# Kernel optimization log

Measured on AMD Instinct MI355X. Metric: run time of the kernel, lower is better.

Reference implementation:

```python
import jax, jax.numpy as jnp
import numpy as np

N, D, H, E = 32768, 1024, 1024, 4


def setup_inputs() -> dict:
    key = jax.random.key(0)
    ks = jax.random.split(key, 10)
    s = 0.02  # xavier-ish init scale for stability
    return {
        "features": jax.random.normal(ks[0], (N, D), dtype=jnp.float32),
        "symbol_ids": jax.random.randint(ks[1], (N,), 0, E, dtype=jnp.int32),
        "W1": jax.random.normal(ks[2], (E, D, H), dtype=jnp.float32) * s,
        "b1": jax.random.normal(ks[3], (E, H), dtype=jnp.float32) * s,
        "W2": jax.random.normal(ks[4], (E, H, H), dtype=jnp.float32) * s,
        "b2": jax.random.normal(ks[5], (E, H), dtype=jnp.float32) * s,
        "W3": jax.random.normal(ks[6], (E, H, 1), dtype=jnp.float32) * s,
        "b3": jax.random.normal(ks[7], (E, 1), dtype=jnp.float32) * s,
        "slope": jax.random.normal(ks[8], (E,), dtype=jnp.float32),
        "intercept": jax.random.normal(ks[9], (E,), dtype=jnp.float32),
    }


def reference(features, symbol_ids, W1, b1, W2, b2, W3, b3, slope, intercept):
    # Run every atom through every expert MLP (E is tiny), then select by symbol.
    # h1: [E, N, H]
    h = jax.nn.relu(jnp.einsum("nd,edh->enh", features, W1) + b1[:, None, :])
    h = jax.nn.relu(jnp.einsum("enh,ehk->enk", h, W2) + b2[:, None, :])
    y = (jnp.einsum("enk,eko->eno", h, W3) + b3[:, None, :])[..., 0]  # [E, N]
    per_atom = slope[:, None] * y + intercept[:, None]                # [E, N]
    sel = symbol_ids[None, :] == jnp.arange(E, dtype=symbol_ids.dtype)[:, None]
    atomic_energies = jnp.sum(jnp.where(sel, per_atom, 0.0), axis=0)  # [N]
    image_energy = jnp.sum(atomic_energies)                           # scalar
    return image_energy
```

## Files before the change

kernel.cpp:

```cpp
#include <hip/hip_runtime.h>
#include <hip/hip_bf16.h>
#include <stdint.h>

#define NATOMS 32768
#define DDIM   1024
#define HDIM   1024
#define ENUM   4
#define MCAP   (NATOMS + ENUM * 128)

typedef unsigned short u16;
typedef unsigned char  u8;
typedef __attribute__((ext_vector_type(8)))  int   i32x8;
typedef __attribute__((ext_vector_type(16))) float f32x16;
typedef __attribute__((ext_vector_type(4)))  float f32x4;

static const size_t XP_OFF   = 0;
static const size_t H1_OFF   = XP_OFF  + (size_t)MCAP * 1024;
static const size_t W1T_OFF  = H1_OFF  + (size_t)MCAP * 1024;
static const size_t W2T_OFF  = W1T_OFF + (size_t)ENUM * 1024 * 1024;
static const size_t PERM_OFF = W2T_OFF + (size_t)ENUM * 1024 * 1024;
static const size_t META_OFF = PERM_OFF + (size_t)MCAP * 4;

__device__ __forceinline__ u8 f2fp8(float x) {
    int w = __builtin_amdgcn_cvt_pk_fp8_f32(x, x, 0, false);
    return (u8)(w & 0xFF);
}

__global__ void k_init(int* __restrict__ perm, int* __restrict__ meta,
                       float* __restrict__ out) {
    int i = blockIdx.x * 256 + threadIdx.x;
    if (i < MCAP) perm[i] = -1;
    if (blockIdx.x == 0) {
        if (threadIdx.x < 256) meta[threadIdx.x] = 0;
        if (threadIdx.x == 0) out[0] = 0.0f;
    }
}

__global__ void k_count(const int* __restrict__ sym, int* __restrict__ meta) {
    int n = blockIdx.x * 256 + threadIdx.x;
    int lane = threadIdx.x & 63;
    int e = sym[n];
#pragma unroll
    for (int j = 0; j < ENUM; ++j) {
        unsigned long long mask = __ballot(e == j);
        if (mask) {
            int leader = __ffsll((long long)mask) - 1;
            if (lane == leader)
                atomicAdd(&meta[j * 16], __popcll(mask));
        }
    }
}

__global__ void k_offsets(int* __restrict__ meta, const float* __restrict__ slope,
                          const float* __restrict__ b3, const float* __restrict__ inter,
                          float* __restrict__ out) {
    if (threadIdx.x == 0 && blockIdx.x == 0) {
        int off = 0;
        float c = 0.f;
        for (int e = 0; e < 4; ++e) {
            meta[128 + e]    = off;
            meta[64 + e*16]  = off;
            int cnt = meta[e * 16];
            c += (float)cnt * (slope[e] * b3[e] + inter[e]);
            off += (cnt + 127) & ~127;
        }
        meta[132] = off;
        out[0] = c;
    }
}

__global__ void k_scatter(const int* __restrict__ sym, int* __restrict__ meta,
                          int* __restrict__ perm) {
    int n = blockIdx.x * 256 + threadIdx.x;
    int lane = threadIdx.x & 63;
    int e = sym[n];
#pragma unroll
    for (int j = 0; j < ENUM; ++j) {
        unsigned long long mask = __ballot(e == j);
        if (mask) {
            int leader = __ffsll((long long)mask) - 1;
            int base = 0;
            if (lane == leader)
                base = atomicAdd(&meta[64 + j * 16], __popcll(mask));
            base = __shfl(base, leader, 64);
            if (e == j) {
                int rank = __popcll(mask & ((1ull << lane) - 1ull));
                perm[base + rank] = n;
            }
        }
    }
}

__global__ void k_convx(const float* __restrict__ F, const int* __restrict__ perm,
                        u8* __restrict__ Xp) {
    int g = blockIdx.x * 256 + threadIdx.x;
    int slot = g >> 7, c = g & 127;
    int src = perm[slot];
    uint2 v;
    if (src < 0) {
        v.x = 0u; v.y = 0u;
    } else {
        const float* fp = F + (size_t)src * 1024 + c * 8;
        int w0 = 0, w1 = 0;
        w0 = __builtin_amdgcn_cvt_pk_fp8_f32(fp[0], fp[1], w0, false);
        w0 = __builtin_amdgcn_cvt_pk_fp8_f32(fp[2], fp[3], w0, true);
        w1 = __builtin_amdgcn_cvt_pk_fp8_f32(fp[4], fp[5], w1, false);
        w1 = __builtin_amdgcn_cvt_pk_fp8_f32(fp[6], fp[7], w1, true);
        v.x = (unsigned)w0; v.y = (unsigned)w1;
    }
    *(uint2*)(void*)(Xp + (size_t)g * 8) = v;
}

__global__ void k_transw(const float* __restrict__ W1, u8* __restrict__ W1T,
                         const float* __restrict__ W2, u8* __restrict__ W2T) {
    __shared__ u8 tile[64][65];
    const float* W  = blockIdx.z ? W2  : W1;
    u8*          WT = blockIdx.z ? W2T : W1T;
    int e  = blockIdx.y;
    int tn = blockIdx.x & 15;
    int tk = blockIdx.x >> 4;
    const float* Wp = W  + (size_t)e * 1024 * 1024;
    u8*         WTp = WT + (size_t)e * 1024 * 1024;
    int c = threadIdx.x & 63, r0 = threadIdx.x >> 6;
#pragma unroll
    for (int i = 0; i < 16; ++i) {
        int r = r0 + i * 4;
        tile[r][c] = f2fp8(32.0f * Wp[(size_t)(tk * 64 + r) * 1024 + tn * 64 + c]);
    }
    __syncthreads();
#pragma unroll
    for (int i = 0; i < 16; ++i) {
        int r = r0 + i * 4;
        WTp[(size_t)(tn * 64 + r) * 1024 + tk * 64 + c] = tile[c][r];
    }
}

template <bool FUSE>
__global__ __launch_bounds__(256, 4)
void k_gemm(const u8* __restrict__ A, const u8* __restrict__ BT,
            const float* __restrict__ bias, u8* __restrict__ C,
            const int* __restrict__ meta, const float* __restrict__ W3,
            const float* __restrict__ slope, float* __restrict__ out) {
    __shared__ u8 As[128 * 64];
    __shared__ u8 Bs[128 * 64];
    const int* offs = meta + 128;

    const int bx = blockIdx.x;
    const int by = blockIdx.y;
    const int m0 = by * 128, n0 = bx * 128;
    int e = (m0 >= offs[1]) + (m0 >= offs[2]) + (m0 >= offs[3]);

    const int t = threadIdx.x;
    const int w = t >> 6, lane = t & 63;
    const int l31 = lane & 31, khalf = lane >> 5;
    const int wm = w & 1, wn = w >> 1;

    const u8* Ag = A + (size_t)m0 * 1024;
    const u8* Bg = BT + (size_t)e * 1024 * 1024 + (size_t)n0 * 1024;

    const int srow   = t >> 2;
    const int gchunk = (t & 3) ^ (srow & 3);

    f32x16 acc[2][2] = {};

    for (int kt = 0; kt < 1024 / 64; ++kt) {
        const int kb = kt * 64;
#pragma unroll
        for (int i = 0; i < 2; ++i) {
            int row = i * 64 + srow;
            __builtin_amdgcn_global_load_lds(
                (const void*)(Ag + (size_t)row * 1024 + kb + gchunk * 16),
                (void*)(As + i * 4096 + w * 1024), 16, 0, 0);
        }
#pragma unroll
        for (int i = 0; i < 2; ++i) {
            int row = i * 64 + srow;
            __builtin_amdgcn_global_load_lds(
                (const void*)(Bg + (size_t)row * 1024 + kb + gchunk * 16),
                (void*)(Bs + i * 4096 + w * 1024), 16, 0, 0);
        }
        __syncthreads();

        i32x8 a[2], b[2];
#pragma unroll
        for (int mi = 0; mi < 2; ++mi) {
            int m = wm * 64 + mi * 32 + l31;
            const u8* base = As + m * 64 + ((khalf ^ ((m >> 1) & 1)) << 5);
            uint4 lo = *(const uint4*)(const void*)(base + ((m & 1) << 4));
            uint4 hi = *(const uint4*)(const void*)(base + (((m & 1) ^ 1) << 4));
            union { uint4 q[2]; i32x8 v; } u;
            u.q[0] = lo; u.q[1] = hi;
            a[mi] = u.v;
        }
#pragma unroll
        for (int ni = 0; ni < 2; ++ni) {
            int n = wn * 64 + ni * 32 + l31;
            const u8* base = Bs + n * 64 + ((khalf ^ ((n >> 1) & 1)) << 5);
            uint4 lo = *(const uint4*)(const void*)(base + ((n & 1) << 4));
            uint4 hi = *(const uint4*)(const void*)(base + (((n & 1) ^ 1) << 4));
            union { uint4 q[2]; i32x8 v; } u;
            u.q[0] = lo; u.q[1] = hi;
            b[ni] = u.v;
        }
#pragma unroll
        for (int mi = 0; mi < 2; ++mi)
#pragma unroll
            for (int ni = 0; ni < 2; ++ni)
                acc[mi][ni] = __builtin_amdgcn_mfma_scale_f32_32x32x64_f8f6f4(
                    a[mi], b[ni], acc[mi][ni],
                    0, 0,
                    0, 0x7F7F7F7F,
                    0, 0x7A7A7A7A);
        __syncthreads();
    }

    if (!FUSE) {
#pragma unroll
        for (int ni = 0; ni < 2; ++ni) {
            int col = n0 + wn * 64 + ni * 32 + l31;
            float bv = bias[e * 1024 + col];
#pragma unroll
            for (int mi = 0; mi < 2; ++mi) {
                int rowb = m0 + wm * 64 + mi * 32 + 4 * khalf;
#pragma unroll
                for (int reg = 0; reg < 16; ++reg) {
                    int rowg = rowb + (reg & 3) + 8 * (reg >> 2);
                    float v = acc[mi][ni][reg] + bv;
                    v = v > 0.f ? v : 0.f;
                    C[(size_t)rowg * 1024 + col] = f2fp8(v);
                }
            }
        }
    } else {
        const int segEnd = offs[e] + meta[e * 16];
        const float se = slope[e];
        float psum = 0.f;
#pragma unroll
        for (int ni = 0; ni < 2; ++ni) {
            int col = n0 + wn * 64 + ni * 32 + l31;
            float bv  = bias[e * 1024 + col];
            float w3s = W3[e * 1024 + col] * se;
#pragma unroll
            for (int mi = 0; mi < 2; ++mi) {
                int rowb = m0 + wm * 64 + mi * 32 + 4 * khalf;
#pragma unroll
                for (int reg = 0; reg < 16; ++reg) {
                    int rowg = rowb + (reg & 3) + 8 * (reg >> 2);
                    float v = acc[mi][ni][reg] + bv;
                    v = v > 0.f ? v : 0.f;
                    psum += (rowg < segEnd) ? v * w3s : 0.f;
                }
            }
        }
#pragma unroll
        for (int o = 32; o; o >>= 1) psum += __shfl_xor(psum, o, 64);
        float* red = (float*)As;
        if (lane == 0) red[w] = psum;
        __syncthreads();
        if (t == 0) atomicAdd(out, red[0] + red[1] + red[2] + red[3]);
    }
}

extern "C" void kernel_launch(void* const* d_in, const int* in_sizes, int n_in,
                              void* d_out, int out_size, void* d_ws, size_t ws_size,
                              hipStream_t stream) {
    const float* features = (const float*)d_in[0];
    const int*   sym      = (const int*)d_in[1];
    const float* W1       = (const float*)d_in[2];
    const float* b1       = (const float*)d_in[3];
    const float* W2       = (const float*)d_in[4];
    const float* b2       = (const float*)d_in[5];
    const float* W3       = (const float*)d_in[6];
    const float* b3       = (const float*)d_in[7];
    const float* slope    = (const float*)d_in[8];
    const float* inter    = (const float*)d_in[9];
    float* out = (float*)d_out;

    char* ws  = (char*)d_ws;
    u8*  Xp   = (u8*)(ws + XP_OFF);
    u8*  H1b  = (u8*)(ws + H1_OFF);
    u8*  W1T  = (u8*)(ws + W1T_OFF);
    u8*  W2T  = (u8*)(ws + W2T_OFF);
    int* perm = (int*)(ws + PERM_OFF);
    int* meta = (int*)(ws + META_OFF);

    k_init<<<MCAP / 256, 256, 0, stream>>>(perm, meta, out);
    k_count<<<NATOMS / 256, 256, 0, stream>>>(sym, meta);
    k_offsets<<<1, 64, 0, stream>>>(meta, slope, b3, inter, out);
    k_scatter<<<NATOMS / 256, 256, 0, stream>>>(sym, meta, perm);
    k_convx<<<(MCAP * 128) / 256, 256, 0, stream>>>(features, perm, Xp);
    k_transw<<<dim3(256, 4, 2), 256, 0, stream>>>(W1, W1T, W2, W2T);
    k_gemm<false><<<dim3(8, 260), 256, 0, stream>>>(Xp, W1T, b1, H1b, meta,
                                                    nullptr, nullptr, nullptr);
    k_gemm<true><<<dim3(8, 260), 256, 0, stream>>>(H1b, W2T, b2, nullptr, meta,
                                                   W3, slope, out);
}
```

Before: 384.9 us.

## Double GEMM K-tile to 128 and group block order for L2 reuse

The FP8 GEMM now stages a 128-wide K slice per iteration instead of 64, halving the number of barrier pairs per tile and issuing two MFMA k-steps per load. LDS swizzle is widened to 8 chunks to match the new row length. Blocks are remapped so groups of 8 M-tiles sweep all N-tiles together, improving L2 reuse of the weight and activation panels, with grid padded to 264 rows and early exit for excess tiles. LDS usage doubles to 32KB per block, which may reduce occupancy under the 4-block launch bound.

```diff
diff --git a/kernel.cpp b/kernel.cpp
--- a/kernel.cpp
+++ b/kernel.cpp
@@ -7,6 +7,7 @@
 #define HDIM   1024
 #define ENUM   4
 #define MCAP   (NATOMS + ENUM * 128)
+#define MTILES 260
 
 typedef unsigned short u16;
 typedef unsigned char  u8;
@@ -141,13 +142,15 @@
             const float* __restrict__ bias, u8* __restrict__ C,
             const int* __restrict__ meta, const float* __restrict__ W3,
             const float* __restrict__ slope, float* __restrict__ out) {
-    __shared__ u8 As[128 * 64];
-    __shared__ u8 Bs[128 * 64];
+    __shared__ u8 As[128 * 128];
+    __shared__ u8 Bs[128 * 128];
     const int* offs = meta + 128;
 
-    const int bx = blockIdx.x;
-    const int by = blockIdx.y;
-    const int m0 = by * 128, n0 = bx * 128;
+    const int flat = blockIdx.y * 8 + blockIdx.x;
+    const int mt = (flat >> 6) * 8 + (flat & 7);
+    const int nt = (flat & 63) >> 3;
+    if (mt >= MTILES) return;
+    const int m0 = mt * 128, n0 = nt * 128;
     int e = (m0 >= offs[1]) + (m0 >= offs[2]) + (m0 >= offs[3]);
 
     const int t = threadIdx.x;
@@ -158,59 +161,65 @@
     const u8* Ag = A + (size_t)m0 * 1024;
     const u8* Bg = BT + (size_t)e * 1024 * 1024 + (size_t)n0 * 1024;
 
-    const int srow   = t >> 2;
-    const int gchunk = (t & 3) ^ (srow & 3);
+    const int srow   = t >> 3;
+    const int gchunk = (t & 7) ^ (srow & 7);
 
     f32x16 acc[2][2] = {};
 
-    for (int kt = 0; kt < 1024 / 64; ++kt) {
-        const int kb = kt * 64;
-#pragma unroll
-        for (int i = 0; i < 2; ++i) {
-            int row = i * 64 + srow;
+    for (int kt = 0; kt < 1024 / 128; ++kt) {
+        const int kb = kt * 128;
+#pragma unroll
+        for (int i = 0; i < 4; ++i) {
+            int row = i * 32 + srow;
             __builtin_amdgcn_global_load_lds(
                 (const void*)(Ag + (size_t)row * 1024 + kb + gchunk * 16),
                 (void*)(As + i * 4096 + w * 1024), 16, 0, 0);
         }
 #pragma unroll
-        for (int i = 0; i < 2; ++i) {
-            int row = i * 64 + srow;
+        for (int i = 0; i < 4; ++i) {
+            int row = i * 32 + srow;
             __builtin_amdgcn_global_load_lds(
                 (const void*)(Bg + (size_t)row * 1024 + kb + gchunk * 16),
                 (void*)(Bs + i * 4096 + w * 1024), 16, 0, 0);
         }
         __syncthreads();
 
-        i32x8 a[2], b[2];
-#pragma unroll
-        for (int mi = 0; mi < 2; ++mi) {
-            int m = wm * 64 + mi * 32 + l31;
-            const u8* base = As + m * 64 + ((khalf ^ ((m >> 1) & 1)) << 5);
-            uint4 lo = *(const uint4*)(const void*)(base + ((m & 1) << 4));
-            uint4 hi = *(const uint4*)(const void*)(base + (((m & 1) ^ 1) << 4));
-            union { uint4 q[2]; i32x8 v; } u;
-            u.q[0] = lo; u.q[1] = hi;
-            a[mi] = u.v;
-        }
-#pragma unroll
-        for (int ni = 0; ni < 2; ++ni) {
-            int n = wn * 64 + ni * 32 + l31;
-            const u8* base = Bs + n * 64 + ((khalf ^ ((n >> 1) & 1)) << 5);
-            uint4 lo = *(const uint4*)(const void*)(base + ((n & 1) << 4));
-            uint4 hi = *(const uint4*)(const void*)(base + (((n & 1) ^ 1) << 4));
-            union { uint4 q[2]; i32x8 v; } u;
-            u.q[0] = lo; u.q[1] = hi;
-            b[ni] = u.v;
-        }
-#pragma unroll
-        for (int mi = 0; mi < 2; ++mi)
-#pragma unroll
-            for (int ni = 0; ni < 2; ++ni)
-                acc[mi][ni] = __builtin_amdgcn_mfma_scale_f32_32x32x64_f8f6f4(
-                    a[mi], b[ni], acc[mi][ni],
-                    0, 0,
-                    0, 0x7F7F7F7F,
-                    0, 0x7A7A7A7A);
+#pragma unroll
+        for (int kk = 0; kk < 2; ++kk) {
+            const int c0 = 4 * kk + 2 * khalf;
+            i32x8 a[2], b[2];
+#pragma unroll
+            for (int mi = 0; mi < 2; ++mi) {
+                int m = wm * 64 + mi * 32 + l31;
+                const u8* base = As + m * 128;
+                int lo = ((c0 ^ (m & 7)) << 4);
+                uint4 q0 = *(const uint4*)(const void*)(base + lo);
+                uint4 q1 = *(const uint4*)(const void*)(base + (lo ^ 16));
+                union { uint4 q[2]; i32x8 v; } u;
+                u.q[0] = q0; u.q[1] = q1;
+                a[mi] = u.v;
+            }
+#pragma unroll
+            for (int ni = 0; ni < 2; ++ni) {
+                int n = wn * 64 + ni * 32 + l31;
+                const u8* base = Bs + n * 128;
+                int lo = ((c0 ^ (n & 7)) << 4);
+                uint4 q0 = *(const uint4*)(const void*)(base + lo);
+                uint4 q1 = *(const uint4*)(const void*)(base + (lo ^ 16));
+                union { uint4 q[2]; i32x8 v; } u;
+                u.q[0] = q0; u.q[1] = q1;
+                b[ni] = u.v;
+            }
+#pragma unroll
+            for (int mi = 0; mi < 2; ++mi)
+#pragma unroll
+                for (int ni = 0; ni < 2; ++ni)
+                    acc[mi][ni] = __builtin_amdgcn_mfma_scale_f32_32x32x64_f8f6f4(
+                        a[mi], b[ni], acc[mi][ni],
+                        0, 0,
+                        0, 0x7F7F7F7F,
+                        0, 0x7A7A7A7A);
+        }
         __syncthreads();
     }
 
@@ -290,8 +299,8 @@
     k_scatter<<<NATOMS / 256, 256, 0, stream>>>(sym, meta, perm);
     k_convx<<<(MCAP * 128) / 256, 256, 0, stream>>>(features, perm, Xp);
     k_transw<<<dim3(256, 4, 2), 256, 0, stream>>>(W1, W1T, W2, W2T);
-    k_gemm<false><<<dim3(8, 260), 256, 0, stream>>>(Xp, W1T, b1, H1b, meta,
+    k_gemm<false><<<dim3(8, 264), 256, 0, stream>>>(Xp, W1T, b1, H1b, meta,
                                                     nullptr, nullptr, nullptr);
-    k_gemm<true><<<dim3(8, 260), 256, 0, stream>>>(H1b, W2T, b2, nullptr, meta,
+    k_gemm<true><<<dim3(8, 264), 256, 0, stream>>>(H1b, W2T, b2, nullptr, meta,
                                                    W3, slope, out);
 }
```

After: 355.8 us. 1.08x faster.
